# Kernel tuning notes

Measured on AMD Instinct MI355X. Metric: run time of the kernel, lower is better.

The kernel has to match this reference:

```python
import jax, jax.numpy as jnp
import numpy as np

N = 20000   # nodes
E = 160000  # edges
IN = 16     # in_channels
H = 32      # hidden_channels
MID = 32    # edge-MLP hidden width


def setup_inputs() -> dict:
    key = jax.random.key(0)
    ks = jax.random.split(key, 18)
    s = 0.1  # param scale
    return {
        "x": jax.random.normal(ks[0], (N, IN), jnp.float32),
        "edge_index": jax.random.randint(ks[1], (2, E), 0, N, dtype=jnp.int64),
        "edge_weight": jax.random.uniform(ks[2], (E,), jnp.float32),
        # edge_net1: Linear(1,32) -> SiLU -> Linear(32, IN*H)
        "en1_w1": jax.random.normal(ks[3], (1, MID), jnp.float32) * s,
        "en1_b1": jax.random.normal(ks[4], (MID,), jnp.float32) * s,
        "en1_w2": jax.random.normal(ks[5], (MID, IN * H), jnp.float32) * s,
        "en1_b2": jax.random.normal(ks[6], (IN * H,), jnp.float32) * s,
        "root1": jax.random.normal(ks[7], (IN, H), jnp.float32) * s,
        "bias1": jax.random.normal(ks[8], (H,), jnp.float32) * s,
        # edge_net2: Linear(1,32) -> SiLU -> Linear(32, H*H)
        "en2_w1": jax.random.normal(ks[9], (1, MID), jnp.float32) * s,
        "en2_b1": jax.random.normal(ks[10], (MID,), jnp.float32) * s,
        "en2_w2": jax.random.normal(ks[11], (MID, H * H), jnp.float32) * s,
        "en2_b2": jax.random.normal(ks[12], (H * H,), jnp.float32) * s,
        "root2": jax.random.normal(ks[13], (H, H), jnp.float32) * s,
        "bias2": jax.random.normal(ks[14], (H,), jnp.float32) * s,
        "dec_w": jax.random.normal(ks[15], (H, 1), jnp.float32) * s,
        "dec_b": jax.random.normal(ks[16], (1,), jnp.float32) * s,
    }


def _nnconv(x, src, dst, inv_cnt, e, w1, b1, w2, b2, root, bias, cin, cout):
    # edge MLP -> per-edge [cin, cout] weight matrix
    h = jax.nn.silu(e @ w1 + b1)            # [E, MID]
    w = (h @ w2 + b2).reshape(-1, cin, cout)  # [E, cin, cout]
    msg = jnp.einsum('ei,eio->eo', x[src], w)  # per-edge matmul [E, cout]
    agg = jax.ops.segment_sum(msg, dst, num_segments=N) * inv_cnt  # scatter-mean
    return agg + x @ root + bias


def reference(x, edge_index, edge_weight,
              en1_w1, en1_b1, en1_w2, en1_b2, root1, bias1,
              en2_w1, en2_b1, en2_w2, en2_b2, root2, bias2,
              dec_w, dec_b):
    src, dst = edge_index[0], edge_index[1]
    e = edge_weight[:, None]  # [E, 1]
    cnt = jax.ops.segment_sum(jnp.ones((E,), x.dtype), dst, num_segments=N)
    inv_cnt = (1.0 / jnp.maximum(cnt, 1.0))[:, None]  # [N, 1]
    h = _nnconv(x, src, dst, inv_cnt, e, en1_w1, en1_b1, en1_w2, en1_b2, root1, bias1, IN, H)
    h = jax.nn.silu(h)
    h = _nnconv(h, src, dst, inv_cnt, e, en2_w1, en2_b1, en2_w2, en2_b2, root2, bias2, H, H)
    h = jax.nn.silu(h)
    out = h @ dec_w + dec_b  # [N, 1]
    return out[:, 0]
```

## Files before the change

### kernel.cpp

```cpp
#include <hip/hip_runtime.h>
#include <hip/hip_bf16.h>

#define NN 20000
#define EE 160000
#define HH 32
#define MIDD 32
#define NB 128
#define EPB 1250

typedef _Float16 f16x4 __attribute__((ext_vector_type(4)));
typedef _Float16 f16x8 __attribute__((ext_vector_type(8)));
typedef float f32x4 __attribute__((ext_vector_type(4)));

__device__ __forceinline__ float silu_f(float v) {
    return __fdividef(v, 1.0f + __expf(-v));
}

__device__ __forceinline__ void gload_lds_b32(const void* gsrc, void* ldst) {
    __builtin_amdgcn_global_load_lds(
        (const __attribute__((address_space(1))) void*)gsrc,
        (__attribute__((address_space(3))) void*)ldst, 4, 0, 0);
}

__device__ __forceinline__ int swz4(int e) { return ((e >> 2) & 3) << 2; }

__global__ __launch_bounds__(256) void prep_kernel(
    const int* __restrict__ ei,
    const float* __restrict__ w2a, const float* __restrict__ b2a,
    const float* __restrict__ ra,
    const float* __restrict__ w2b, const float* __restrict__ b2b,
    const float* __restrict__ rb,
    const float* __restrict__ x,
    unsigned int* __restrict__ histG,
    _Float16* __restrict__ Wt1, _Float16* __restrict__ Wt2,
    _Float16* __restrict__ x16) {
    const int t = threadIdx.x;
    if (blockIdx.x < NB) {
        __shared__ unsigned int h2[NN / 2];
        for (int i = t; i < NN / 2; i += 256) h2[i] = 0u;
        __syncthreads();
        const int base = blockIdx.x * EPB;
        for (int e = base + t; e < base + EPB; e += 256) {
            int d = ei[EE + e];
            atomicAdd(&h2[d >> 1], 1u << ((d & 1) * 16));
        }
        __syncthreads();
        unsigned int* outp = histG + (size_t)blockIdx.x * NN;
        for (int n = t; n < NN; n += 256)
            outp[n] = (h2[n >> 1] >> ((n & 1) * 16)) & 0xFFFFu;
        return;
    }
    int idx = (blockIdx.x - NB) * 256 + t;
    if (idx < 17408) {
        int o = idx / 544, k = idx % 544;
        float v;
        if (k < 512) {
            int m = k & 31, i = k >> 5;
            v = w2a[m * 512 + i * 32 + o];
        } else if (k < 528) {
            v = b2a[(k - 512) * 32 + o];
        } else {
            v = ra[(k - 528) * 32 + o];
        }
        Wt1[o * 544 + k] = (_Float16)v;
    } else if (idx < 52224) {
        int j = idx - 17408;
        int o = j / 1088, k = j % 1088;
        float v;
        if (k < 1024) {
            int m = k & 31, i = k >> 5;
            v = w2b[m * 1024 + i * 32 + o];
        } else if (k < 1056) {
            v = b2b[(k - 1024) * 32 + o];
        } else {
            v = rb[(k - 1056) * 32 + o];
        }
        Wt2[o * 1088 + k] = (_Float16)v;
    } else if (idx < 52224 + NN * 16) {
        int j = idx - 52224;
        x16[j] = (_Float16)x[j];
    }
}

__global__ __launch_bounds__(256) void colscan_kernel(
    unsigned int* __restrict__ histG, int* __restrict__ cnt,
    float* __restrict__ invc) {
    const int n = blockIdx.x * 256 + threadIdx.x;
    if (n >= NN) return;
    unsigned int s = 0;
    #pragma unroll 4
    for (int b = 0; b < NB; ++b) {
        unsigned int v = histG[(size_t)b * NN + n];
        histG[(size_t)b * NN + n] = s;
        s += v;
    }
    cnt[n] = (int)s;
    invc[n] = 1.0f / fmaxf((float)s, 1.0f);
}

__global__ __launch_bounds__(1024) void scan_kernel(
    const int* __restrict__ cnt, int* __restrict__ off) {
    const int t = threadIdx.x;
    const int base = t * 20;
    __shared__ int wtot[16];

    int c[20];
    if (base + 20 <= NN) {
        const int4* p = (const int4*)(cnt + base);
        #pragma unroll
        for (int q = 0; q < 5; ++q) *(int4*)&c[4 * q] = p[q];
    } else {
        #pragma unroll
        for (int r = 0; r < 20; ++r) {
            int idx = base + r;
            c[r] = (idx < NN) ? cnt[idx] : 0;
        }
    }

    int loc[20];
    int s = 0;
    #pragma unroll
    for (int r = 0; r < 20; ++r) { loc[r] = s; s += c[r]; }

    const int lane = t & 63, wv = t >> 6;
    int incl = s;
    #pragma unroll
    for (int d2 = 1; d2 < 64; d2 <<= 1) {
        int u = __shfl_up(incl, d2);
        if (lane >= d2) incl += u;
    }
    if (lane == 63) wtot[wv] = incl;
    __syncthreads();
    int wbase = 0;
    for (int p2 = 0; p2 < wv; ++p2) wbase += wtot[p2];

    const int excl = wbase + incl - s;

    int o[20];
    #pragma unroll
    for (int r = 0; r < 20; ++r) o[r] = excl + loc[r];

    if (base + 20 <= NN) {
        #pragma unroll
        for (int q = 0; q < 5; ++q)
            ((int4*)(off + base))[q] = *(const int4*)&o[4 * q];
    } else {
        #pragma unroll
        for (int r = 0; r < 20; ++r) {
            int idx = base + r;
            if (idx < NN) off[idx] = o[r];
        }
    }
    if (t == 0) off[NN] = EE;
}

__global__ __launch_bounds__(256) void scatter2_kernel(
    const int* __restrict__ ei, const float* __restrict__ ewt,
    const int* __restrict__ off, const unsigned int* __restrict__ histG,
    int2* __restrict__ spair) {
    __shared__ unsigned int r2[NN / 2];
    const int t = threadIdx.x, b = blockIdx.x;
    for (int i = t; i < NN / 2; i += 256) r2[i] = 0u;
    __syncthreads();
    const int base = b * EPB;
    const unsigned int* hb = histG + (size_t)b * NN;
    for (int e = base + t; e < base + EPB; e += 256) {
        int d = ei[EE + e];
        unsigned int old = atomicAdd(&r2[d >> 1], 1u << ((d & 1) * 16));
        int rank = (int)((old >> ((d & 1) * 16)) & 0xFFFFu);
        int pos = off[d] + (int)hb[d] + rank;
        spair[pos] = make_int2(ei[e], __float_as_int(ewt[e]));
    }
}


template <int CIN, bool DECODE>
__global__ __launch_bounds__(512, 4) void fused_layer(
    const _Float16* __restrict__ xin16, const int* __restrict__ spair,
    const int* __restrict__ off, const float* __restrict__ invc,
    const float* __restrict__ w1, const float* __restrict__ b1,
    const _Float16* __restrict__ Wt, const float* __restrict__ bias,
    void* __restrict__ outp, const float* __restrict__ dw,
    const float* __restrict__ db) {
    constexpr int K = 34 * CIN;
    constexpr int LDK = K + 4;
    constexpr int steps = K / 32;
    constexpr int CAP = 192;
    constexpr int RPG = 128 / CIN;
    constexpr int LPR = CIN / 2;
    constexpr int NIH = CIN / 16;

    extern __shared__ char smem[];
    _Float16* Fl = (_Float16*)smem;
    char* poolb = smem + (size_t)16 * LDK * 2;
    int* Ps = (int*)poolb;
    _Float16* Xs = (_Float16*)(poolb + (2 * CAP + 64) * 4);
    _Float16* Hs = Xs + CAP * CIN;
    float* red = (float*)poolb;

    const int t = threadIdx.x;
    const int n0 = blockIdx.x * 16;
    const int lane = t & 63, w = t >> 6;
    const int col = lane & 15, g4 = (lane >> 4) * 4;
    const int qcl = col & 1, qhi = col >> 1;

    const int E0 = off[n0], E1 = off[n0 + 16];
    const int L = E1 - E0;

    const int d0 = n0 + w * 2;
    const int e0l0 = off[d0] - E0;
    const int e1l0 = off[d0 + 1] - E0;
    const int e1l1 = off[d0 + 2] - E0;

    const float w1v = w1[t & 31];
    const float b1v = b1[t & 31];

    f32x4 aS[2][2][NIH];
    f32x4 a0[2][NIH];
    #pragma unroll
    for (int c = 0; c < 2; ++c) {
        #pragma unroll
        for (int mh = 0; mh < 2; ++mh)
            #pragma unroll
            for (int ih = 0; ih < NIH; ++ih) aS[c][mh][ih] = (f32x4){0.f, 0.f, 0.f, 0.f};
        #pragma unroll
        for (int ih = 0; ih < NIH; ++ih) a0[c][ih] = (f32x4){0.f, 0.f, 0.f, 0.f};
    }

    for (int base = 0; base < L; base += CAP) {
        const int Lc = (L - base < CAP) ? (L - base) : CAP;

        for (int c = w * 64; c < 2 * Lc; c += 512) {
            int gidx = 2 * (E0 + base) + c + lane;
            gidx = (gidx < 2 * EE) ? gidx : (2 * EE - 1);
            gload_lds_b32(spair + gidx, Ps + c);
        }
        __syncthreads();

        {
            const int G = (Lc + RPG - 1) / RPG;
            const int er = lane / LPR, ecp = lane % LPR;
            for (int p = w; p < G; p += 8) {
                int el = p * RPG + er; el = (el < Lc - 1) ? el : (Lc - 1);
                int sn = Ps[2 * el];
                int sp = (CIN == 32) ? (ecp ^ swz4(el)) : ecp;
                gload_lds_b32(xin16 + (size_t)sn * CIN + 2 * sp,
                              Xs + (size_t)p * RPG * CIN);
            }
        }
        for (int idx = t; idx < Lc * 32; idx += 512) {
            int e = idx >> 5, m = idx & 31;
            float ew = __int_as_float(Ps[2 * e + 1]);
            int slot = (((m >> 1) ^ swz4(e)) << 1) + (m & 1);
            Hs[e * 32 + slot] = (_Float16)silu_f(fmaf(ew, w1v, b1v));
        }
        __syncthreads();

        #pragma unroll
        for (int c = 0; c < 2; ++c) {
            int lo = ((c == 0) ? e0l0 : e1l0) - base;
            int hi = ((c == 0) ? e1l0 : e1l1) - base;
            lo = (lo < 0) ? 0 : lo;
            hi = (hi > Lc) ? Lc : hi;
            for (int ks = lo; ks < hi; ks += 32) {
                f16x8 bf[NIH];
                #pragma unroll
                for (int ih = 0; ih < NIH; ++ih) {
                    const int qx = ih * 8 + qhi;
                    #pragma unroll
                    for (int j = 0; j < 4; ++j) {
                        int k1 = ks + g4 + j, k2 = k1 + 16;
                        int c1 = (k1 < hi) ? k1 : (Lc - 1);
                        int c2 = (k2 < hi) ? k2 : (Lc - 1);
                        if (CIN == 32) {
                            bf[ih][j]     = Xs[c1 * 32 + ((qx ^ swz4(c1)) << 1) + qcl];
                            bf[ih][j + 4] = Xs[c2 * 32 + ((qx ^ swz4(c2)) << 1) + qcl];
                        } else {
                            bf[ih][j]     = Xs[c1 * CIN + ih * 16 + col];
                            bf[ih][j + 4] = Xs[c2 * CIN + ih * 16 + col];
                        }
                    }
                }
                f16x8 af[2];
                #pragma unroll
                for (int mh = 0; mh < 2; ++mh) {
                    const int qh = mh * 8 + qhi;
                    #pragma unroll
                    for (int j = 0; j < 4; ++j) {
                        int k1 = ks + g4 + j, k2 = k1 + 16;
                        int c1 = (k1 < hi) ? k1 : (Lc - 1);
                        int c2 = (k2 < hi) ? k2 : (Lc - 1);
                        _Float16 v1 = Hs[c1 * 32 + ((qh ^ swz4(c1)) << 1) + qcl];
                        _Float16 v2 = Hs[c2 * 32 + ((qh ^ swz4(c2)) << 1) + qcl];
                        af[mh][j]     = (k1 < hi) ? v1 : (_Float16)0;
                        af[mh][j + 4] = (k2 < hi) ? v2 : (_Float16)0;
                    }
                }
                f16x8 ao;
                #pragma unroll
                for (int j = 0; j < 4; ++j) {
                    int k1 = ks + g4 + j, k2 = k1 + 16;
                    ao[j]     = (col == 0 && k1 < hi) ? (_Float16)1 : (_Float16)0;
                    ao[j + 4] = (col == 0 && k2 < hi) ? (_Float16)1 : (_Float16)0;
                }
                #pragma unroll
                for (int mh = 0; mh < 2; ++mh)
                    #pragma unroll
                    for (int ih = 0; ih < NIH; ++ih)
                        aS[c][mh][ih] = __builtin_amdgcn_mfma_f32_16x16x32_f16(
                            af[mh], bf[ih], aS[c][mh][ih], 0, 0, 0);
                #pragma unroll
                for (int ih = 0; ih < NIH; ++ih)
                    a0[c][ih] = __builtin_amdgcn_mfma_f32_16x16x32_f16(
                        ao, bf[ih], a0[c][ih], 0, 0, 0);
            }
        }
        if (base + CAP < L) __syncthreads();
    }

    #pragma unroll
    for (int c = 0; c < 2; ++c) {
        const int d = n0 + w * 2 + c;
        const float iv = invc[d];
        _Float16* Fr = Fl + (size_t)(w * 2 + c) * LDK;
        #pragma unroll
        for (int mh = 0; mh < 2; ++mh)
            #pragma unroll
            for (int ih = 0; ih < NIH; ++ih)
                #pragma unroll
                for (int r = 0; r < 4; ++r)
                    Fr[32 * (ih * 16 + col) + mh * 16 + g4 + r] =
                        (_Float16)(aS[c][mh][ih][r] * iv);
        if (g4 == 0) {
            #pragma unroll
            for (int ih = 0; ih < NIH; ++ih)
                Fr[32 * CIN + ih * 16 + col] = (_Float16)(a0[c][ih][0] * iv);
        }
        if (lane >= CIN && lane < 2 * CIN)
            Fr[32 * CIN + lane] = xin16[(size_t)d * CIN + (lane - CIN)];
    }
    __syncthreads();

    const int o16 = col, g = lane >> 4;

    const _Float16* Arow = Fl + (size_t)o16 * LDK + g * 4;
    const _Float16* B0 = Wt + (size_t)o16 * K + g * 4;
    const _Float16* B1 = Wt + (size_t)(o16 + 16) * K + g * 4;

    f32x4 acc0 = {0.f, 0.f, 0.f, 0.f};
    f32x4 acc1 = {0.f, 0.f, 0.f, 0.f};

    const int sb = (steps * w) >> 3;
    const int se = (steps * (w + 1)) >> 3;
    #pragma unroll 2
    for (int s = sb; s < se; ++s) {
        const int k0 = s * 32;
        f16x4 alo = *(const f16x4*)(Arow + k0);
        f16x4 ahi = *(const f16x4*)(Arow + k0 + 16);
        f16x4 b0l = *(const f16x4*)(B0 + k0);
        f16x4 b0h = *(const f16x4*)(B0 + k0 + 16);
        f16x4 b1l = *(const f16x4*)(B1 + k0);
        f16x4 b1h = *(const f16x4*)(B1 + k0 + 16);
        f16x8 a, bb0, bb1;
        #pragma unroll
        for (int j = 0; j < 4; ++j) {
            a[j] = alo[j];  a[j + 4] = ahi[j];
            bb0[j] = b0l[j]; bb0[j + 4] = b0h[j];
            bb1[j] = b1l[j]; bb1[j + 4] = b1h[j];
        }
        acc0 = __builtin_amdgcn_mfma_f32_16x16x32_f16(a, bb0, acc0, 0, 0, 0);
        acc1 = __builtin_amdgcn_mfma_f32_16x16x32_f16(a, bb1, acc1, 0, 0, 0);
    }

    if (w > 0) {
        float* rw = red + (w - 1) * 512;
        #pragma unroll
        for (int r = 0; r < 4; ++r) {
            rw[(g * 4 + r) * 32 + o16]      = acc0[r];
            rw[(g * 4 + r) * 32 + 16 + o16] = acc1[r];
        }
    }
    __syncthreads();
    if (w == 0) {
        #pragma unroll
        for (int r = 0; r < 4; ++r) {
            const int ro = (g * 4 + r) * 32 + o16;
            #pragma unroll
            for (int p = 0; p < 7; ++p) {
                acc0[r] += red[p * 512 + ro];
                acc1[r] += red[p * 512 + ro + 16];
            }
        }
        const float bb0 = bias[o16], bb1 = bias[o16 + 16];
        const int nrow = n0 + g * 4;
        if (!DECODE) {
            _Float16* op = (_Float16*)outp;
            #pragma unroll
            for (int r = 0; r < 4; ++r) {
                op[(size_t)(nrow + r) * 32 + o16]      = (_Float16)silu_f(acc0[r] + bb0);
                op[(size_t)(nrow + r) * 32 + 16 + o16] = (_Float16)silu_f(acc1[r] + bb1);
            }
        } else {
            float* op = (float*)outp;
            const float w0 = dw[o16], w1vv = dw[o16 + 16];
            const float dbv = db[0];
            #pragma unroll
            for (int r = 0; r < 4; ++r) {
                float p = silu_f(acc0[r] + bb0) * w0 + silu_f(acc1[r] + bb1) * w1vv;
                p += __shfl_xor(p, 1);
                p += __shfl_xor(p, 2);
                p += __shfl_xor(p, 4);
                p += __shfl_xor(p, 8);
                if (o16 == 0) op[nrow + r] = p + dbv;
            }
        }
    }
}


extern "C" void kernel_launch(void* const* d_in, const int* in_sizes, int n_in,
                              void* d_out, int out_size, void* d_ws, size_t ws_size,
                              hipStream_t stream) {
    const float* x      = (const float*)d_in[0];
    const int*   ei     = (const int*)d_in[1];
    const float* ew     = (const float*)d_in[2];
    const float* en1_w1 = (const float*)d_in[3];
    const float* en1_b1 = (const float*)d_in[4];
    const float* en1_w2 = (const float*)d_in[5];
    const float* en1_b2 = (const float*)d_in[6];
    const float* root1  = (const float*)d_in[7];
    const float* bias1  = (const float*)d_in[8];
    const float* en2_w1 = (const float*)d_in[9];
    const float* en2_b1 = (const float*)d_in[10];
    const float* en2_w2 = (const float*)d_in[11];
    const float* en2_b2 = (const float*)d_in[12];
    const float* root2  = (const float*)d_in[13];
    const float* bias2  = (const float*)d_in[14];
    const float* dec_w  = (const float*)d_in[15];
    const float* dec_b  = (const float*)d_in[16];
    float* out = (float*)d_out;
    (void)in_sizes; (void)n_in; (void)out_size; (void)ws_size;

    char* wp = (char*)d_ws;
    auto alloc = [&](size_t bytes) {
        char* p = wp;
        wp += (bytes + 255) & ~(size_t)255;
        return p;
    };
    unsigned int* histG = (unsigned int*)alloc((size_t)NB * NN * 4);
    int*      cnt   = (int*)alloc((size_t)NN * 4);
    int*      off   = (int*)alloc((size_t)(NN + 1) * 4);
    float*    invc  = (float*)alloc((size_t)NN * 4);
    int2*     spair = (int2*)alloc((size_t)EE * 8);
    _Float16* h1h   = (_Float16*)alloc((size_t)NN * 32 * 2);
    _Float16* x16   = (_Float16*)alloc((size_t)NN * 16 * 2);
    _Float16* Wt1   = (_Float16*)alloc((size_t)17408 * 2);
    _Float16* Wt2   = (_Float16*)alloc((size_t)34816 * 2);

    const int build_blocks = (52224 + NN * 16 + 255) / 256;
    prep_kernel<<<NB + build_blocks, 256, 0, stream>>>(
        ei, en1_w2, en1_b2, root1, en2_w2, en2_b2, root2, x,
        histG, Wt1, Wt2, x16);
    colscan_kernel<<<(NN + 255) / 256, 256, 0, stream>>>(histG, cnt, invc);
    scan_kernel<<<1, 1024, 0, stream>>>(cnt, off);
    scatter2_kernel<<<NB, 256, 0, stream>>>(ei, ew, off, histG, spair);

    auto f1 = fused_layer<16, false>;
    auto f2 = fused_layer<32, true>;
    (void)hipFuncSetAttribute((const void*)f1,
                              hipFuncAttributeMaxDynamicSharedMemorySize, 163840);
    (void)hipFuncSetAttribute((const void*)f2,
                              hipFuncAttributeMaxDynamicSharedMemorySize, 163840);

    const size_t lds1 = (size_t)16 * (34 * 16 + 4) * 2 + (448 * 4 + 192 * 16 * 2 + 192 * 64);
    const size_t lds2 = (size_t)16 * (34 * 32 + 4) * 2 + (448 * 4 + 192 * 32 * 2 + 192 * 64);

    fused_layer<16, false><<<NN / 16, 512, lds1, stream>>>(
        x16, (const int*)spair, off, invc, en1_w1, en1_b1, Wt1, bias1, h1h,
        nullptr, nullptr);
    fused_layer<32, true><<<NN / 16, 512, lds2, stream>>>(
        h1h, (const int*)spair, off, invc, en2_w1, en2_b1, Wt2, bias2, out,
        dec_w, dec_b);
}
```

Baseline: 98.68 us.

## Fuse column scan with offset scan via last-block atomic and halve histogram blocks

Merges the column-scan and single-block prefix-scan kernels into one launch. A global atomic counter, reset in the prep kernel, picks the last block to finish, and that block computes the node offsets over 80 nodes per thread. It also halves the number of edge-partition blocks (NB 128 to 64), which shrinks the per-block histogram and the column-scan loop. The cost is less parallelism in the histogram and scatter kernels, plus a serial tail inside the last block.

```diff
diff --git a/kernel.cpp b/kernel.cpp
--- a/kernel.cpp
+++ b/kernel.cpp
@@ -5,8 +5,8 @@
 #define EE 160000
 #define HH 32
 #define MIDD 32
-#define NB 128
-#define EPB 1250
+#define NB 64
+#define EPB 2500
 
 typedef _Float16 f16x4 __attribute__((ext_vector_type(4)));
 typedef _Float16 f16x8 __attribute__((ext_vector_type(8)));
@@ -33,7 +33,7 @@
     const float* __restrict__ x,
     unsigned int* __restrict__ histG,
     _Float16* __restrict__ Wt1, _Float16* __restrict__ Wt2,
-    _Float16* __restrict__ x16) {
+    _Float16* __restrict__ x16, int* __restrict__ flag) {
     const int t = threadIdx.x;
     if (blockIdx.x < NB) {
         __shared__ unsigned int h2[NN / 2];
@@ -50,6 +50,7 @@
             outp[n] = (h2[n >> 1] >> ((n & 1) * 16)) & 0xFFFFu;
         return;
     }
+    if (blockIdx.x == NB && t == 0) *flag = 0;
     int idx = (blockIdx.x - NB) * 256 + t;
     if (idx < 17408) {
         int o = idx / 544, k = idx % 544;
@@ -82,46 +83,39 @@
     }
 }
 
-__global__ __launch_bounds__(256) void colscan_kernel(
+__global__ __launch_bounds__(256) void colscan_scan_kernel(
     unsigned int* __restrict__ histG, int* __restrict__ cnt,
-    float* __restrict__ invc) {
+    float* __restrict__ invc, int* __restrict__ off, int* __restrict__ flag) {
     const int n = blockIdx.x * 256 + threadIdx.x;
-    if (n >= NN) return;
-    unsigned int s = 0;
-    #pragma unroll 4
-    for (int b = 0; b < NB; ++b) {
-        unsigned int v = histG[(size_t)b * NN + n];
-        histG[(size_t)b * NN + n] = s;
-        s += v;
-    }
-    cnt[n] = (int)s;
-    invc[n] = 1.0f / fmaxf((float)s, 1.0f);
-}
-
-__global__ __launch_bounds__(1024) void scan_kernel(
-    const int* __restrict__ cnt, int* __restrict__ off) {
+    if (n < NN) {
+        unsigned int s = 0;
+        #pragma unroll 4
+        for (int b = 0; b < NB; ++b) {
+            unsigned int v = histG[(size_t)b * NN + n];
+            histG[(size_t)b * NN + n] = s;
+            s += v;
+        }
+        cnt[n] = (int)s;
+        invc[n] = 1.0f / fmaxf((float)s, 1.0f);
+    }
+    __threadfence();
+    __shared__ int isLast;
+    __shared__ int wtot[4];
+    if (threadIdx.x == 0)
+        isLast = (atomicAdd(flag, 1) == (int)gridDim.x - 1) ? 1 : 0;
+    __syncthreads();
+    if (!isLast) return;
+
     const int t = threadIdx.x;
-    const int base = t * 20;
-    __shared__ int wtot[16];
-
-    int c[20];
-    if (base + 20 <= NN) {
-        const int4* p = (const int4*)(cnt + base);
-        #pragma unroll
-        for (int q = 0; q < 5; ++q) *(int4*)&c[4 * q] = p[q];
-    } else {
-        #pragma unroll
-        for (int r = 0; r < 20; ++r) {
-            int idx = base + r;
-            c[r] = (idx < NN) ? cnt[idx] : 0;
-        }
-    }
-
-    int loc[20];
+    const int base = t * 80;
     int s = 0;
-    #pragma unroll
-    for (int r = 0; r < 20; ++r) { loc[r] = s; s += c[r]; }
-
+    if (base + 80 <= NN) {
+        #pragma unroll
+        for (int q = 0; q < 20; ++q) {
+            int4 v = ((const int4*)(cnt + base))[q];
+            s += v.x + v.y + v.z + v.w;
+        }
+    }
     const int lane = t & 63, wv = t >> 6;
     int incl = s;
     #pragma unroll
@@ -133,22 +127,18 @@
     __syncthreads();
     int wbase = 0;
     for (int p2 = 0; p2 < wv; ++p2) wbase += wtot[p2];
-
-    const int excl = wbase + incl - s;
-
-    int o[20];
-    #pragma unroll
-    for (int r = 0; r < 20; ++r) o[r] = excl + loc[r];
-
-    if (base + 20 <= NN) {
-        #pragma unroll
-        for (int q = 0; q < 5; ++q)
-            ((int4*)(off + base))[q] = *(const int4*)&o[4 * q];
-    } else {
-        #pragma unroll
-        for (int r = 0; r < 20; ++r) {
-            int idx = base + r;
-            if (idx < NN) off[idx] = o[r];
+    int running = wbase + incl - s;
+    if (base + 80 <= NN) {
+        #pragma unroll
+        for (int q = 0; q < 20; ++q) {
+            int4 v = ((const int4*)(cnt + base))[q];
+            int4 o;
+            o.x = running;
+            o.y = running + v.x;
+            o.z = o.y + v.y;
+            o.w = o.z + v.z;
+            ((int4*)(off + base))[q] = o;
+            running = o.w + v.w;
         }
     }
     if (t == 0) off[NN] = EE;
@@ -456,13 +446,14 @@
     _Float16* x16   = (_Float16*)alloc((size_t)NN * 16 * 2);
     _Float16* Wt1   = (_Float16*)alloc((size_t)17408 * 2);
     _Float16* Wt2   = (_Float16*)alloc((size_t)34816 * 2);
+    int*      flag  = (int*)alloc(256);
 
     const int build_blocks = (52224 + NN * 16 + 255) / 256;
     prep_kernel<<<NB + build_blocks, 256, 0, stream>>>(
         ei, en1_w2, en1_b2, root1, en2_w2, en2_b2, root2, x,
-        histG, Wt1, Wt2, x16);
-    colscan_kernel<<<(NN + 255) / 256, 256, 0, stream>>>(histG, cnt, invc);
-    scan_kernel<<<1, 1024, 0, stream>>>(cnt, off);
+        histG, Wt1, Wt2, x16, flag);
+    colscan_scan_kernel<<<(NN + 255) / 256, 256, 0, stream>>>(
+        histG, cnt, invc, off, flag);
     scatter2_kernel<<<NB, 256, 0, stream>>>(ei, ew, off, histG, spair);
 
     auto f1 = fused_layer<16, false>;
```

Result: slower. 104.7 us (+6.1%).
